# Performance work log

Measured on AMD Instinct MI355X. Metric: run time of the kernel, lower is better.

## Reference

```python
import jax, jax.numpy as jnp
import numpy as np

N, E, D, H = 50000, 800000, 128, 4

def setup_inputs() -> dict:
    key = jax.random.key(0)
    ks = jax.random.split(key, 6)
    x = jax.random.normal(ks[0], (N, D), dtype=jnp.float32)
    edge_index = jax.random.randint(ks[1], (2, E), 0, N, dtype=jnp.int64)
    W = jax.random.normal(ks[2], (D, H * D), dtype=jnp.float32) * (1.0 / np.sqrt(D))
    att_src = jax.random.normal(ks[3], (H, D), dtype=jnp.float32) * 0.1
    att_dst = jax.random.normal(ks[4], (H, D), dtype=jnp.float32) * 0.1
    bias = jnp.zeros((D,), dtype=jnp.float32)
    gamma = jnp.ones((D,), dtype=jnp.float32)
    beta = jnp.zeros((D,), dtype=jnp.float32)
    return {"x": x, "edge_index": edge_index, "W": W, "att_src": att_src,
            "att_dst": att_dst, "bias": bias, "gamma": gamma, "beta": beta}

def reference(x, edge_index, W, att_src, att_dst, bias, gamma, beta):
    src, dst = edge_index[0], edge_index[1]
    # GATConv: linear transform per head -> [N, H, D]
    xw = (x @ W).reshape(N, H, D)
    a_src = jnp.einsum('nhd,hd->nh', xw, att_src)  # [N, H]
    a_dst = jnp.einsum('nhd,hd->nh', xw, att_dst)  # [N, H]
    alpha = a_src[src] + a_dst[dst]                # [E, H]
    alpha = jax.nn.leaky_relu(alpha, negative_slope=0.2)
    # segment softmax over incoming edges of each dst node
    m = jax.ops.segment_max(alpha, dst, num_segments=N)   # [N, H]
    ex = jnp.exp(alpha - m[dst])                            # [E, H]
    denom = jax.ops.segment_sum(ex, dst, num_segments=N)   # [N, H]
    attn = ex / denom[dst]                                  # [E, H]
    msg = xw[src] * attn[:, :, None]                        # [E, H, D]
    agg = jax.ops.segment_sum(msg, dst, num_segments=N)    # [N, H, D]
    out = agg.mean(axis=1) + bias                           # concat=False: mean heads
    # LayerNorm (eps=1e-5)
    mu = out.mean(axis=-1, keepdims=True)
    var = out.var(axis=-1, keepdims=True)
    out = (out - mu) * jax.lax.rsqrt(var + 1e-5) * gamma + beta
    out = jax.nn.gelu(out, approximate=False)
    return out + x  # project is Identity (in_channels == out_channels)
```

## Files before the change

### kernel.cpp

```cpp
#include <hip/hip_runtime.h>
#include <hip/hip_bf16.h>
#include <hip/hip_fp16.h>
#include <math.h>

#define ND 128
#define NH 4
#define HD 512

typedef __attribute__((ext_vector_type(8))) short bf16x8;
typedef __attribute__((ext_vector_type(4))) float f32x4;

__device__ __forceinline__ unsigned pack_bf16(float a, float b) {
    unsigned ua = __float_as_uint(a), ub = __float_as_uint(b);
    ua = (ua + 0x7fffu + ((ua >> 16) & 1u)) >> 16;
    ub = (ub + 0x7fffu + ((ub >> 16) & 1u)) >> 16;
    return ua | (ub << 16);
}
__device__ __forceinline__ unsigned short bf16r(float a) {
    unsigned ua = __float_as_uint(a);
    return (unsigned short)((ua + 0x7fffu + ((ua >> 16) & 1u)) >> 16);
}
__device__ __forceinline__ float bflo(unsigned u) { return __uint_as_float(u << 16); }
__device__ __forceinline__ float bfhi(unsigned u) { return __uint_as_float(u & 0xffff0000u); }

__device__ __forceinline__ unsigned pack_half2(float a, float b) {
    __half ha = __float2half(a), hb = __float2half(b);
    return (unsigned)__half_as_ushort(ha) | ((unsigned)__half_as_ushort(hb) << 16);
}

__global__ __launch_bounds__(256) void prep_and_hist(const float* __restrict__ W,
                                                     unsigned short* __restrict__ Wt,
                                                     const int* __restrict__ dst,
                                                     int* __restrict__ cnt, int ne) {
    if (blockIdx.x < 256) {
        int idx = blockIdx.x * 256 + threadIdx.x;
        int nl = idx >> 7, k = idx & 127;
        Wt[idx] = bf16r(W[(size_t)k * HD + nl]);
    } else {
        int e = (blockIdx.x - 256) * 256 + threadIdx.x;
        if (e < ne) atomicAdd(&cnt[dst[e]], 1);
    }
}

__global__ __launch_bounds__(256, 2) void gemm_mfma(
        const float* __restrict__ x, const unsigned short* __restrict__ Wt,
        const float* __restrict__ att_src, const float* __restrict__ att_dst,
        unsigned short* __restrict__ xw, float* __restrict__ a_src,
        float* __restrict__ a_dst, int n) {
    __shared__ char lds[65536];
    char* As = lds;
    char* Bs = lds + 32768;
    const int t = threadIdx.x;
    const int row0 = blockIdx.x * 128;
    const int l = t & 63, w = t >> 6;
    const int eid = l & 15, g = l >> 4;

#pragma unroll
    for (int i = 0; i < 8; ++i) {
        int c = t + i * 256;
        int m = c >> 4, kb = c & 15;
        int row = row0 + m;
        uint4 pk;
        if (row < n) {
            const float4* xp = (const float4*)(x + (size_t)row * ND + kb * 8);
            float4 f0 = xp[0], f1 = xp[1];
            pk.x = pack_bf16(f0.x, f0.y); pk.y = pack_bf16(f0.z, f0.w);
            pk.z = pack_bf16(f1.x, f1.y); pk.w = pack_bf16(f1.z, f1.w);
        } else { pk.x = pk.y = pk.z = pk.w = 0u; }
        *(uint4*)(As + m * 256 + ((kb * 16) ^ ((m & 7) << 4))) = pk;
    }

    for (int hh = 0; hh < 2; ++hh) {
        const int h = blockIdx.y * 2 + hh;
        __syncthreads();
#pragma unroll
        for (int i = 0; i < 8; ++i) {
            int c = t + i * 256;
            int nl = c >> 4, kb = c & 15;
            uint4 pv = *(const uint4*)(Wt + (size_t)(h * 128 + nl) * 128 + kb * 8);
            *(uint4*)(Bs + nl * 256 + ((kb * 16) ^ ((nl & 7) << 4))) = pv;
        }
        __syncthreads();

        f32x4 acc[2][8];
#pragma unroll
        for (int mt = 0; mt < 2; ++mt)
#pragma unroll
            for (int nr = 0; nr < 8; ++nr) acc[mt][nr] = (f32x4){0.f, 0.f, 0.f, 0.f};

        const int swz = (eid & 7) << 4;
#pragma unroll
        for (int ks = 0; ks < 4; ++ks) {
            int koff = (ks * 64 + g * 16) ^ swz;
            bf16x8 a0 = *(const bf16x8*)(As + (w * 32 + eid) * 256 + koff);
            bf16x8 a1 = *(const bf16x8*)(As + (w * 32 + 16 + eid) * 256 + koff);
#pragma unroll
            for (int nr = 0; nr < 8; ++nr) {
                bf16x8 b = *(const bf16x8*)(Bs + (nr * 16 + eid) * 256 + koff);
                acc[0][nr] = __builtin_amdgcn_mfma_f32_16x16x32_bf16(a0, b, acc[0][nr], 0, 0, 0);
                acc[1][nr] = __builtin_amdgcn_mfma_f32_16x16x32_bf16(a1, b, acc[1][nr], 0, 0, 0);
            }
        }

        float asv[8], adv[8];
#pragma unroll
        for (int nr = 0; nr < 8; ++nr) {
            asv[nr] = att_src[h * ND + nr * 16 + eid];
            adv[nr] = att_dst[h * ND + nr * 16 + eid];
        }
#pragma unroll
        for (int mt = 0; mt < 2; ++mt) {
#pragma unroll
            for (int ri = 0; ri < 4; ++ri) {
                float s = 0.f, d = 0.f;
#pragma unroll
                for (int nr = 0; nr < 8; ++nr) {
                    s += acc[mt][nr][ri] * asv[nr];
                    d += acc[mt][nr][ri] * adv[nr];
                }
#pragma unroll
                for (int off = 1; off < 16; off <<= 1) {
                    s += __shfl_xor(s, off);
                    d += __shfl_xor(d, off);
                }
                int row = row0 + w * 32 + mt * 16 + g * 4 + ri;
                if (eid == 0 && row < n) {
                    a_src[(size_t)row * NH + h] = s;
                    a_dst[(size_t)row * NH + h] = d;
                }
            }
        }

        __syncthreads();
        unsigned short* Ps = (unsigned short*)Bs;
#pragma unroll
        for (int mt = 0; mt < 2; ++mt)
#pragma unroll
            for (int ri = 0; ri < 4; ++ri) {
                int rl = w * 32 + mt * 16 + g * 4 + ri;
#pragma unroll
                for (int nr = 0; nr < 8; ++nr)
                    Ps[rl * 128 + nr * 16 + eid] = bf16r(acc[mt][nr][ri]);
            }
        __syncthreads();
#pragma unroll
        for (int i = 0; i < 8; ++i) {
            int row = i * 16 + (t >> 4);
            int grow = row0 + row;
            if (grow < n) {
                uint4 v = *(const uint4*)(Ps + row * 128 + (t & 15) * 8);
                *(uint4*)(xw + (size_t)grow * HD + h * ND + (t & 15) * 8) = v;
            }
        }
    }
}

__global__ __launch_bounds__(256) void scanA(const int* __restrict__ cnt,
                                             int* __restrict__ partial,
                                             int* __restrict__ bsum, int n) {
    __shared__ int sh[256];
    int gid = blockIdx.x * 256 + threadIdx.x;
    int v = (gid < n) ? cnt[gid] : 0;
    int val = v;
    sh[threadIdx.x] = val;
    __syncthreads();
#pragma unroll
    for (int off = 1; off < 256; off <<= 1) {
        int add = (threadIdx.x >= off) ? sh[threadIdx.x - off] : 0;
        __syncthreads();
        val += add;
        sh[threadIdx.x] = val;
        __syncthreads();
    }
    if (gid < n) partial[gid] = val - v;
    if (threadIdx.x == 255) bsum[blockIdx.x] = val;
}

__global__ __launch_bounds__(256) void scanB(int* __restrict__ bsum, int nb) {
    __shared__ int sh[256];
    int t = threadIdx.x;
    int v = (t < nb) ? bsum[t] : 0;
    int val = v;
    sh[t] = val;
    __syncthreads();
#pragma unroll
    for (int off = 1; off < 256; off <<= 1) {
        int add = (t >= off) ? sh[t - off] : 0;
        __syncthreads();
        val += add;
        sh[t] = val;
        __syncthreads();
    }
    if (t < nb) bsum[t] = val - v;
}

__global__ __launch_bounds__(256) void scanC(const int* __restrict__ partial,
                                             const int* __restrict__ bsum,
                                             int* __restrict__ starts,
                                             int* __restrict__ cursor, int n, int ne) {
    int gid = blockIdx.x * 256 + threadIdx.x;
    if (gid < n) {
        int s = partial[gid] + bsum[blockIdx.x];
        starts[gid] = s;
        cursor[gid] = s;
    }
    if (gid == 0) starts[n] = ne;
}

__global__ __launch_bounds__(256) void scatter_edges_w(const int* __restrict__ src,
                                                       const int* __restrict__ dst,
                                                       const float* __restrict__ a_src,
                                                       const float* __restrict__ a_dst,
                                                       int* __restrict__ cursor,
                                                       uint4* __restrict__ eperm, int ne) {
    int e = blockIdx.x * 256 + threadIdx.x;
    if (e < ne) {
        int s = src[e], t = dst[e];
        float4 as = *(const float4*)(a_src + (size_t)s * NH);
        float4 ad = *(const float4*)(a_dst + (size_t)t * NH);
        float A0 = as.x + ad.x, A1 = as.y + ad.y, A2 = as.z + ad.z, A3 = as.w + ad.w;
        A0 = (A0 > 0.f) ? A0 : 0.2f * A0;
        A1 = (A1 > 0.f) ? A1 : 0.2f * A1;
        A2 = (A2 > 0.f) ? A2 : 0.2f * A2;
        A3 = (A3 > 0.f) ? A3 : 0.2f * A3;
        float e0 = expf(A0), e1 = expf(A1), e2 = expf(A2), e3 = expf(A3);
        int pos = atomicAdd(&cursor[t], 1);
        uint4 ev;
        ev.x = (unsigned)s;
        ev.y = pack_half2(e0, e1);
        ev.z = pack_half2(e2, e3);
        ev.w = 0u;
        eperm[pos] = ev;
    }
}

#define ACC8(vv, ww)                                                      \
    acc[0] = fmaf(ww, bflo(vv.x), acc[0]);                                \
    acc[1] = fmaf(ww, bfhi(vv.x), acc[1]);                                \
    acc[2] = fmaf(ww, bflo(vv.y), acc[2]);                                \
    acc[3] = fmaf(ww, bfhi(vv.y), acc[3]);                                \
    acc[4] = fmaf(ww, bflo(vv.z), acc[4]);                                \
    acc[5] = fmaf(ww, bfhi(vv.z), acc[5]);                                \
    acc[6] = fmaf(ww, bflo(vv.w), acc[6]);                                \
    acc[7] = fmaf(ww, bfhi(vv.w), acc[7]);

__global__ __launch_bounds__(256) void node_agg(const uint4* __restrict__ eperm,
                                                const int* __restrict__ starts,
                                                const uint4* __restrict__ xw,
                                                const float* __restrict__ x,
                                                const float* __restrict__ bias,
                                                const float* __restrict__ gamma,
                                                const float* __restrict__ beta,
                                                float* __restrict__ out, int n) {
    int node = (blockIdx.x * 256 + threadIdx.x) >> 6;
    int lane = threadIdx.x & 63;
    if (node >= n) return;
    const int hgrp = lane >> 4;
    const int eid = lane & 15;
    const int hb = hgrp << 4;

    int s0 = starts[node], s1 = starts[node + 1];

    float den = 0.f;
    float acc[8];
#pragma unroll
    for (int j = 0; j < 8; ++j) acc[j] = 0.f;

    for (int base = s0; base < s1; base += 16) {
        int rem = s1 - base; if (rem > 16) rem = 16;
        int sl = 0; float em = 0.f;
        if (eid < rem) {
            uint4 ev = eperm[base + eid];
            sl = (int)ev.x;
            unsigned wb = (hgrp & 2) ? ev.z : ev.y;
            unsigned short hbits = (hgrp & 1) ? (unsigned short)(wb >> 16)
                                              : (unsigned short)(wb & 0xffffu);
            em = __half2float(__ushort_as_half(hbits));
        }
        den += em;

        int jj = 0;
        for (; jj + 4 <= rem; jj += 4) {
            int t0 = __shfl(sl, jj),     t1 = __shfl(sl, jj + 1);
            int t2 = __shfl(sl, jj + 2), t3 = __shfl(sl, jj + 3);
            uint4 v0 = xw[(size_t)t0 * 64 + lane];
            uint4 v1 = xw[(size_t)t1 * 64 + lane];
            uint4 v2 = xw[(size_t)t2 * 64 + lane];
            uint4 v3 = xw[(size_t)t3 * 64 + lane];
            float w0 = __shfl(em, hb + jj);
            float w1 = __shfl(em, hb + jj + 1);
            float w2 = __shfl(em, hb + jj + 2);
            float w3 = __shfl(em, hb + jj + 3);
            ACC8(v0, w0); ACC8(v1, w1); ACC8(v2, w2); ACC8(v3, w3);
        }
        for (; jj < rem; ++jj) {
            int ts = __shfl(sl, jj);
            uint4 v = xw[(size_t)ts * 64 + lane];
            float ww = __shfl(em, hb + jj);
            ACC8(v, ww);
        }
    }

#pragma unroll
    for (int off = 1; off < 16; off <<= 1) den += __shfl_xor(den, off);
    float imy = (den > 0.f) ? 0.25f / den : 0.f;

    float v[8];
#pragma unroll
    for (int j = 0; j < 8; ++j) {
        v[j] = acc[j] * imy;
        v[j] += __shfl_xor(v[j], 16);
        v[j] += __shfl_xor(v[j], 32);
    }

    const float4* bp = (const float4*)(bias + eid * 8);
    float4 b0 = bp[0], b1 = bp[1];
    v[0] += b0.x; v[1] += b0.y; v[2] += b0.z; v[3] += b0.w;
    v[4] += b1.x; v[5] += b1.y; v[6] += b1.z; v[7] += b1.w;

    float s = 0.f, s2 = 0.f;
#pragma unroll
    for (int j = 0; j < 8; ++j) { s += v[j]; s2 += v[j] * v[j]; }
#pragma unroll
    for (int off = 1; off < 16; off <<= 1) {
        s += __shfl_xor(s, off);
        s2 += __shfl_xor(s2, off);
    }
    float mu = s * (1.0f / ND);
    float var = s2 * (1.0f / ND) - mu * mu;
    var = fmaxf(var, 0.0f);
    float inv = rsqrtf(var + 1e-5f);

    const float4* gp = (const float4*)(gamma + eid * 8);
    const float4* btp = (const float4*)(beta + eid * 8);
    float4 g0 = gp[0], g1 = gp[1];
    float4 t0 = btp[0], t1 = btp[1];
    float gm[8] = {g0.x, g0.y, g0.z, g0.w, g1.x, g1.y, g1.z, g1.w};
    float bt[8] = {t0.x, t0.y, t0.z, t0.w, t1.x, t1.y, t1.z, t1.w};

    float y[8];
#pragma unroll
    for (int j = 0; j < 8; ++j) {
        float yn = (v[j] - mu) * inv * gm[j] + bt[j];
        y[j] = 0.5f * yn * (1.0f + erff(yn * 0.70710678118654752f));
    }

    if (lane < 16) {
        const float4* xp = (const float4*)(x + (size_t)node * ND + eid * 8);
        float4 r0 = xp[0], r1 = xp[1];
        float4 o0 = {y[0] + r0.x, y[1] + r0.y, y[2] + r0.z, y[3] + r0.w};
        float4 o1 = {y[4] + r1.x, y[5] + r1.y, y[6] + r1.z, y[7] + r1.w};
        float4* op = (float4*)(out + (size_t)node * ND + eid * 8);
        op[0] = o0; op[1] = o1;
    }
}

extern "C" void kernel_launch(void* const* d_in, const int* in_sizes, int n_in,
                              void* d_out, int out_size, void* d_ws, size_t ws_size,
                              hipStream_t stream) {
    const float* x       = (const float*)d_in[0];
    const int*   edge    = (const int*)d_in[1];
    const float* W       = (const float*)d_in[2];
    const float* att_src = (const float*)d_in[3];
    const float* att_dst = (const float*)d_in[4];
    const float* bias    = (const float*)d_in[5];
    const float* gamma   = (const float*)d_in[6];
    const float* beta    = (const float*)d_in[7];
    float* out = (float*)d_out;

    const int n  = in_sizes[0] / ND;
    const int ne = in_sizes[1] / 2;
    const int* src = edge;
    const int* dst = edge + ne;

    const int nb = (n + 255) / 256;

    char* wsp = (char*)d_ws;
    unsigned short* xw = (unsigned short*)wsp;  wsp += (size_t)n * HD * sizeof(short);
    unsigned short* Wt = (unsigned short*)wsp;  wsp += (size_t)HD * ND * sizeof(short);
    float* a_src   = (float*)wsp;               wsp += (size_t)n * NH * sizeof(float);
    float* a_dst   = (float*)wsp;               wsp += (size_t)n * NH * sizeof(float);
    uint4* eperm   = (uint4*)wsp;               wsp += (size_t)ne * sizeof(uint4);
    int*   cnt     = (int*)wsp;                 wsp += (size_t)n * sizeof(int);
    int*   partial = (int*)wsp;                 wsp += (size_t)n * sizeof(int);
    int*   bsum    = (int*)wsp;                 wsp += 256 * sizeof(int);
    int*   starts  = (int*)wsp;                 wsp += (size_t)(n + 1) * sizeof(int);
    int*   cursor  = (int*)wsp;                 wsp += (size_t)n * sizeof(int);

    hipMemsetAsync(cnt, 0, (size_t)n * sizeof(int), stream);

    prep_and_hist<<<256 + (ne + 255) / 256, 256, 0, stream>>>(W, Wt, dst, cnt, ne);

    dim3 ggrid((n + 127) / 128, 2);
    gemm_mfma<<<ggrid, 256, 0, stream>>>(x, Wt, att_src, att_dst, xw, a_src, a_dst, n);

    scanA<<<nb, 256, 0, stream>>>(cnt, partial, bsum, n);
    scanB<<<1, 256, 0, stream>>>(bsum, nb);
    scanC<<<nb, 256, 0, stream>>>(partial, bsum, starts, cursor, n, ne);
    scatter_edges_w<<<(ne + 255) / 256, 256, 0, stream>>>(src, dst, a_src, a_dst,
                                                          cursor, eperm, ne);

    node_agg<<<((size_t)n * 64 + 255) / 256, 256, 0, stream>>>(
        eperm, starts, (const uint4*)xw, x, bias, gamma, beta, out, n);
}
```

Before: 241.9 us.

## Split node aggregation across two wavefronts and fuse scan passes

The aggregation now gives each node two wavefronts, each covering two heads. Lanes load 8-byte chunks and walk 32 edges per batch, and the two halves are combined through shared memory before LayerNorm, GELU and the residual. The goal is more parallelism and memory-level concurrency per node, at the cost of a block-wide sync, lighter loads per lane, idle lanes in the epilogue, and twice as many edge-list reads. Separately, the second and third prefix-scan kernels are merged: every block redundantly scans the block sums, which removes one launch.

```diff
diff --git a/kernel.cpp b/kernel.cpp
--- a/kernel.cpp
+++ b/kernel.cpp
@@ -176,7 +176,11 @@
     if (threadIdx.x == 255) bsum[blockIdx.x] = val;
 }
 
-__global__ __launch_bounds__(256) void scanB(int* __restrict__ bsum, int nb) {
+__global__ __launch_bounds__(256) void scanBC(const int* __restrict__ partial,
+                                              const int* __restrict__ bsum,
+                                              int* __restrict__ starts,
+                                              int* __restrict__ cursor,
+                                              int n, int ne, int nb) {
     __shared__ int sh[256];
     int t = threadIdx.x;
     int v = (t < nb) ? bsum[t] : 0;
@@ -191,16 +195,10 @@
         sh[t] = val;
         __syncthreads();
     }
-    if (t < nb) bsum[t] = val - v;
-}
-
-__global__ __launch_bounds__(256) void scanC(const int* __restrict__ partial,
-                                             const int* __restrict__ bsum,
-                                             int* __restrict__ starts,
-                                             int* __restrict__ cursor, int n, int ne) {
-    int gid = blockIdx.x * 256 + threadIdx.x;
+    int myoff = (blockIdx.x == 0) ? 0 : sh[blockIdx.x - 1];
+    int gid = blockIdx.x * 256 + t;
     if (gid < n) {
-        int s = partial[gid] + bsum[blockIdx.x];
+        int s = partial[gid] + myoff;
         starts[gid] = s;
         cursor[gid] = s;
     }
@@ -234,47 +232,48 @@
     }
 }
 
-#define ACC8(vv, ww)                                                      \
+#define ACC4(vv, ww)                                                      \
     acc[0] = fmaf(ww, bflo(vv.x), acc[0]);                                \
     acc[1] = fmaf(ww, bfhi(vv.x), acc[1]);                                \
     acc[2] = fmaf(ww, bflo(vv.y), acc[2]);                                \
-    acc[3] = fmaf(ww, bfhi(vv.y), acc[3]);                                \
-    acc[4] = fmaf(ww, bflo(vv.z), acc[4]);                                \
-    acc[5] = fmaf(ww, bfhi(vv.z), acc[5]);                                \
-    acc[6] = fmaf(ww, bflo(vv.w), acc[6]);                                \
-    acc[7] = fmaf(ww, bfhi(vv.w), acc[7]);
+    acc[3] = fmaf(ww, bfhi(vv.y), acc[3]);
 
 __global__ __launch_bounds__(256) void node_agg(const uint4* __restrict__ eperm,
                                                 const int* __restrict__ starts,
-                                                const uint4* __restrict__ xw,
+                                                const uint2* __restrict__ xw2,
                                                 const float* __restrict__ x,
                                                 const float* __restrict__ bias,
                                                 const float* __restrict__ gamma,
                                                 const float* __restrict__ beta,
                                                 float* __restrict__ out, int n) {
-    int node = (blockIdx.x * 256 + threadIdx.x) >> 6;
-    int lane = threadIdx.x & 63;
-    if (node >= n) return;
-    const int hgrp = lane >> 4;
-    const int eid = lane & 15;
-    const int hb = hgrp << 4;
-
-    int s0 = starts[node], s1 = starts[node + 1];
+    __shared__ float comb[2][32][4];
+
+    const int wib = threadIdx.x >> 6;
+    const int lane = threadIdx.x & 63;
+    const int pairslot = wib >> 1;
+    const int q = wib & 1;
+    const int node = blockIdx.x * 2 + pairslot;
+    const int hsel = lane >> 5;
+    const int slot = lane & 31;
+    const int habs = q * 2 + hsel;
+    const int hb = hsel << 5;
+
+    const bool alive = (node < n);
+    int s0 = 0, s1 = 0;
+    if (alive) { s0 = starts[node]; s1 = starts[node + 1]; }
 
     float den = 0.f;
-    float acc[8];
-#pragma unroll
-    for (int j = 0; j < 8; ++j) acc[j] = 0.f;
-
-    for (int base = s0; base < s1; base += 16) {
-        int rem = s1 - base; if (rem > 16) rem = 16;
+    float acc[4] = {0.f, 0.f, 0.f, 0.f};
+
+    for (int base = s0; base < s1; base += 32) {
+        int rem = s1 - base; if (rem > 32) rem = 32;
         int sl = 0; float em = 0.f;
-        if (eid < rem) {
-            uint4 ev = eperm[base + eid];
+        if (slot < rem) {
+            uint4 ev = eperm[base + slot];
             sl = (int)ev.x;
-            unsigned wb = (hgrp & 2) ? ev.z : ev.y;
-            unsigned short hbits = (hgrp & 1) ? (unsigned short)(wb >> 16)
-                                              : (unsigned short)(wb & 0xffffu);
+            unsigned wb2 = (habs & 2) ? ev.z : ev.y;
+            unsigned short hbits = (habs & 1) ? (unsigned short)(wb2 >> 16)
+                                              : (unsigned short)(wb2 & 0xffffu);
             em = __half2float(__ushort_as_half(hbits));
         }
         den += em;
@@ -283,46 +282,51 @@
         for (; jj + 4 <= rem; jj += 4) {
             int t0 = __shfl(sl, jj),     t1 = __shfl(sl, jj + 1);
             int t2 = __shfl(sl, jj + 2), t3 = __shfl(sl, jj + 3);
-            uint4 v0 = xw[(size_t)t0 * 64 + lane];
-            uint4 v1 = xw[(size_t)t1 * 64 + lane];
-            uint4 v2 = xw[(size_t)t2 * 64 + lane];
-            uint4 v3 = xw[(size_t)t3 * 64 + lane];
+            uint2 v0 = xw2[(size_t)t0 * 128 + habs * 32 + slot];
+            uint2 v1 = xw2[(size_t)t1 * 128 + habs * 32 + slot];
+            uint2 v2 = xw2[(size_t)t2 * 128 + habs * 32 + slot];
+            uint2 v3 = xw2[(size_t)t3 * 128 + habs * 32 + slot];
             float w0 = __shfl(em, hb + jj);
             float w1 = __shfl(em, hb + jj + 1);
             float w2 = __shfl(em, hb + jj + 2);
             float w3 = __shfl(em, hb + jj + 3);
-            ACC8(v0, w0); ACC8(v1, w1); ACC8(v2, w2); ACC8(v3, w3);
+            ACC4(v0, w0); ACC4(v1, w1); ACC4(v2, w2); ACC4(v3, w3);
         }
         for (; jj < rem; ++jj) {
             int ts = __shfl(sl, jj);
-            uint4 v = xw[(size_t)ts * 64 + lane];
+            uint2 v = xw2[(size_t)ts * 128 + habs * 32 + slot];
             float ww = __shfl(em, hb + jj);
-            ACC8(v, ww);
-        }
-    }
-
-#pragma unroll
-    for (int off = 1; off < 16; off <<= 1) den += __shfl_xor(den, off);
+            ACC4(v, ww);
+        }
+    }
+
+#pragma unroll
+    for (int off = 1; off < 32; off <<= 1) den += __shfl_xor(den, off);
     float imy = (den > 0.f) ? 0.25f / den : 0.f;
 
-    float v[8];
-#pragma unroll
-    for (int j = 0; j < 8; ++j) {
+    float v[4];
+#pragma unroll
+    for (int j = 0; j < 4; ++j) {
         v[j] = acc[j] * imy;
-        v[j] += __shfl_xor(v[j], 16);
         v[j] += __shfl_xor(v[j], 32);
     }
 
-    const float4* bp = (const float4*)(bias + eid * 8);
-    float4 b0 = bp[0], b1 = bp[1];
-    v[0] += b0.x; v[1] += b0.y; v[2] += b0.z; v[3] += b0.w;
-    v[4] += b1.x; v[5] += b1.y; v[6] += b1.z; v[7] += b1.w;
-
-    float s = 0.f, s2 = 0.f;
-#pragma unroll
-    for (int j = 0; j < 8; ++j) { s += v[j]; s2 += v[j] * v[j]; }
-#pragma unroll
-    for (int off = 1; off < 16; off <<= 1) {
+    if (q == 1 && lane < 32) {
+#pragma unroll
+        for (int j = 0; j < 4; ++j) comb[pairslot][slot][j] = v[j];
+    }
+    __syncthreads();
+    if (q == 1 || !alive || lane >= 32) return;
+#pragma unroll
+    for (int j = 0; j < 4; ++j) v[j] += comb[pairslot][slot][j];
+
+    float4 bv = *(const float4*)(bias + slot * 4);
+    v[0] += bv.x; v[1] += bv.y; v[2] += bv.z; v[3] += bv.w;
+
+    float s = v[0] + v[1] + v[2] + v[3];
+    float s2 = v[0] * v[0] + v[1] * v[1] + v[2] * v[2] + v[3] * v[3];
+#pragma unroll
+    for (int off = 1; off < 32; off <<= 1) {
         s += __shfl_xor(s, off);
         s2 += __shfl_xor(s2, off);
     }
@@ -331,28 +335,22 @@
     var = fmaxf(var, 0.0f);
     float inv = rsqrtf(var + 1e-5f);
 
-    const float4* gp = (const float4*)(gamma + eid * 8);
-    const float4* btp = (const float4*)(beta + eid * 8);
-    float4 g0 = gp[0], g1 = gp[1];
-    float4 t0 = btp[0], t1 = btp[1];
-    float gm[8] = {g0.x, g0.y, g0.z, g0.w, g1.x, g1.y, g1.z, g1.w};
-    float bt[8] = {t0.x, t0.y, t0.z, t0.w, t1.x, t1.y, t1.z, t1.w};
-
-    float y[8];
-#pragma unroll
-    for (int j = 0; j < 8; ++j) {
+    float4 gv = *(const float4*)(gamma + slot * 4);
+    float4 tv = *(const float4*)(beta + slot * 4);
+    float gm[4] = {gv.x, gv.y, gv.z, gv.w};
+    float bt[4] = {tv.x, tv.y, tv.z, tv.w};
+
+    float4 rv = *(const float4*)(x + (size_t)node * ND + slot * 4);
+    float rs[4] = {rv.x, rv.y, rv.z, rv.w};
+
+    float y[4];
+#pragma unroll
+    for (int j = 0; j < 4; ++j) {
         float yn = (v[j] - mu) * inv * gm[j] + bt[j];
-        y[j] = 0.5f * yn * (1.0f + erff(yn * 0.70710678118654752f));
-    }
-
-    if (lane < 16) {
-        const float4* xp = (const float4*)(x + (size_t)node * ND + eid * 8);
-        float4 r0 = xp[0], r1 = xp[1];
-        float4 o0 = {y[0] + r0.x, y[1] + r0.y, y[2] + r0.z, y[3] + r0.w};
-        float4 o1 = {y[4] + r1.x, y[5] + r1.y, y[6] + r1.z, y[7] + r1.w};
-        float4* op = (float4*)(out + (size_t)node * ND + eid * 8);
-        op[0] = o0; op[1] = o1;
-    }
+        y[j] = 0.5f * yn * (1.0f + erff(yn * 0.70710678118654752f)) + rs[j];
+    }
+    float4 ov = {y[0], y[1], y[2], y[3]};
+    *(float4*)(out + (size_t)node * ND + slot * 4) = ov;
 }
 
 extern "C" void kernel_launch(void* const* d_in, const int* in_sizes, int n_in,
@@ -395,11 +393,10 @@
     gemm_mfma<<<ggrid, 256, 0, stream>>>(x, Wt, att_src, att_dst, xw, a_src, a_dst, n);
 
     scanA<<<nb, 256, 0, stream>>>(cnt, partial, bsum, n);
-    scanB<<<1, 256, 0, stream>>>(bsum, nb);
-    scanC<<<nb, 256, 0, stream>>>(partial, bsum, starts, cursor, n, ne);
+    scanBC<<<nb, 256, 0, stream>>>(partial, bsum, starts, cursor, n, ne, nb);
     scatter_edges_w<<<(ne + 255) / 256, 256, 0, stream>>>(src, dst, a_src, a_dst,
                                                           cursor, eperm, ne);
 
-    node_agg<<<((size_t)n * 64 + 255) / 256, 256, 0, stream>>>(
-        eperm, starts, (const uint4*)xw, x, bias, gamma, beta, out, n);
-}
+    node_agg<<<(n + 1) / 2, 256, 0, stream>>>(
+        eperm, starts, (const uint2*)xw, x, bias, gamma, beta, out, n);
+}
```

Result: no change. 239.2 us (-1.1%).
